# Optimization experiments

Measured on AMD Instinct MI355X. Metric: run time of the kernel, lower is better.

Reference implementation:

```python
import jax, jax.numpy as jnp
import numpy as np

B, N, DIM = 8, 8192, 512
H, DH = 8, 64
INNER = H * DH
EPS = 1e-5


def setup_inputs() -> dict:
    key = jax.random.key(0)
    ks = jax.random.split(key, 5)
    x = jax.random.normal(ks[0], (B, N, DIM), dtype=jnp.float32)
    w_qkv = jax.random.normal(ks[1], (DIM, 3 * INNER), dtype=jnp.float32) * (DIM ** -0.5)
    ln_w = jnp.ones((INNER,), dtype=jnp.float32)
    ln_b = jnp.zeros((INNER,), dtype=jnp.float32)
    w_out = jax.random.normal(ks[2], (INNER, DIM), dtype=jnp.float32) * (INNER ** -0.5)
    b_out = jnp.zeros((DIM,), dtype=jnp.float32)
    return {"x": x, "w_qkv": w_qkv, "ln_w": ln_w, "ln_b": ln_b,
            "w_out": w_out, "b_out": b_out}


def _layernorm(x, w, b):
    mu = jnp.mean(x, axis=-1, keepdims=True)
    var = jnp.mean(jnp.square(x - mu), axis=-1, keepdims=True)
    return (x - mu) * jax.lax.rsqrt(var + EPS) * w + b


def reference(x, w_qkv, ln_w, ln_b, w_out, b_out):
    b, n, _ = x.shape
    qkv = x @ w_qkv  # [b, n, 3*inner]
    q, k, v = jnp.split(qkv, 3, axis=-1)
    # b n (h d) -> b h n d
    def heads(t):
        return t.reshape(b, n, H, DH).transpose(0, 2, 1, 3)
    q, k, v = heads(q), heads(k), heads(v)
    q = jax.nn.relu(q)
    k = jax.nn.relu(k)
    kv = jnp.einsum('bhnm,bhnd->bhmd', k, v)   # [b, h, d, d]
    out = jnp.einsum('bhnm,bhmd->bhnd', q, kv)  # [b, h, n, d]
    out = out.transpose(0, 2, 1, 3).reshape(b, n, INNER)
    out = _layernorm(out, ln_w, ln_b)
    return out @ w_out + b_out
```

## Files before the change

kernel.cpp:

```cpp
#include <hip/hip_runtime.h>
#include <stdint.h>

#define B_ 8
#define N_ 8192
#define DIM_ 512
#define H_ 8
#define DH_ 64
#define ROWS (B_*N_)
#define TRIPLE (3*DIM_)
#define EPS_ 1e-5f
#define PLANE ((size_t)ROWS * 64)

typedef __attribute__((ext_vector_type(8))) short short8;
typedef __attribute__((ext_vector_type(4))) float f32x4;
typedef __attribute__((ext_vector_type(4))) float fl4;
typedef __attribute__((ext_vector_type(4))) unsigned short us4;
typedef __attribute__((ext_vector_type(8))) unsigned short us8;

#define AS1 __attribute__((address_space(1)))
#define AS3 __attribute__((address_space(3)))

__device__ __forceinline__ void gld16(const void* g, void* l) {
    __builtin_amdgcn_global_load_lds((const AS1 void*)(uintptr_t)g,
                                     (AS3 void*)(unsigned)(uintptr_t)l, 16, 0, 0);
}

__device__ inline unsigned short f2bf(float f) {
    union { float f; unsigned int u; } x; x.f = f;
    unsigned int r = x.u + 0x7fffu + ((x.u >> 16) & 1u);
    return (unsigned short)(r >> 16);
}
__device__ inline float bf2f(unsigned short b) {
    union { unsigned int u; float f; } x; x.u = ((unsigned int)b) << 16;
    return x.f;
}

__device__ __forceinline__ int eoff(int row, int col) {
    return row * 64 + (col ^ ((((unsigned)row >> 2) & 3) << 4));
}

__device__ __forceinline__ int aoff(int row, int col) {
    return row * 512 + ((((col >> 3) ^ (row & 7)) << 3) | (col & 7));
}

__global__ __launch_bounds__(256) void k_cvt(const float* __restrict__ x,
                                             unsigned short* __restrict__ xb) {
    size_t i = ((size_t)blockIdx.x * 256 + threadIdx.x) * 8;
    fl4 a = *(const fl4*)(x + i);
    fl4 b = *(const fl4*)(x + i + 4);
    us8 r;
    r[0] = f2bf(a[0]); r[1] = f2bf(a[1]); r[2] = f2bf(a[2]); r[3] = f2bf(a[3]);
    r[4] = f2bf(b[0]); r[5] = f2bf(b[1]); r[6] = f2bf(b[2]); r[7] = f2bf(b[3]);
    *(us8*)(xb + i) = r;
}

__global__ __launch_bounds__(256) void k_prep(const float* __restrict__ wq,
        const float* __restrict__ wo,
        unsigned short* __restrict__ wqT, unsigned short* __restrict__ woT) {
    __shared__ float T[32][33];
    int bid = blockIdx.x;
    const float* src; unsigned short* dst; int srcCols, dstCols, k0, n0;
    if (bid < 768) {
        int tn = bid % 48, tk = bid / 48;
        src = wq; dst = wqT; srcCols = 1536; dstCols = 512;
        k0 = tk * 32; n0 = tn * 32;
    } else {
        int b = bid - 768;
        int tn = b % 16, tk = b / 16;
        src = wo; dst = woT; srcCols = 512; dstCols = 512;
        k0 = tk * 32; n0 = tn * 32;
    }
    int t = threadIdx.x, r = t >> 3, c4 = (t & 7) * 4;
    fl4 v = *(const fl4*)(src + (size_t)(k0 + r) * srcCols + n0 + c4);
    T[c4 + 0][r] = v[0]; T[c4 + 1][r] = v[1];
    T[c4 + 2][r] = v[2]; T[c4 + 3][r] = v[3];
    __syncthreads();
    us4 o;
    o[0] = f2bf(T[r][c4 + 0]); o[1] = f2bf(T[r][c4 + 1]);
    o[2] = f2bf(T[r][c4 + 2]); o[3] = f2bf(T[r][c4 + 3]);
    *(us4*)(dst + (size_t)(n0 + r) * dstCols + k0 + c4) = o;
}

__global__ __launch_bounds__(512, 4) void k_qkv8(const unsigned short* __restrict__ xb,
        const unsigned short* __restrict__ wT,
        unsigned short* __restrict__ qkv)
{
    __shared__ __align__(1024) unsigned short LDSb[3][12288];

    const int tid  = threadIdx.x;
    const int lane = tid & 63;
    const int wid  = tid >> 6;
    const int wr   = wid >> 1;
    const int wc   = wid & 1;
    const int lr   = lane & 15;

    int id  = blockIdx.x;
    int nid = (id & 7) * 384 + (id >> 3);
    int n0  = (nid % 12) * 128;
    int m0  = (nid / 12) * 256;

    const unsigned short* pA[2];
    const unsigned short* pB1;
    unsigned ldstA[2], ldstB;
#pragma unroll
    for (int j = 0; j < 2; ++j) {
        int s    = tid + j * 512;
        int row  = ((s >> 6) << 4) + ((s >> 2) & 15);
        int colb = ((s & 3) << 4) ^ (((s >> 5) & 1) << 5);
        pA[j] = xb + (size_t)(m0 + row) * 512 + (colb >> 1);
        ldstA[j] = (unsigned)((j * 512 + wid * 64) * 8);
    }
    {
        int s    = tid;
        int row  = ((s >> 6) << 4) + ((s >> 2) & 15);
        int colb = ((s & 3) << 4) ^ (((s >> 5) & 1) << 5);
        pB1 = wT + (size_t)(n0 + row) * 512 + (colb >> 1);
        ldstB = (unsigned)(8192 + wid * 64 * 8);
    }
    const int kg = (lane >> 4) * 8;
    const int lo = lr * 32 + (kg ^ ((lr >> 3) << 4));

    auto STAGE = [&](int t, int slot) {
        gld16(pA[0] + t * 32, (void*)&LDSb[slot][ldstA[0]]);
        gld16(pA[1] + t * 32, (void*)&LDSb[slot][ldstA[1]]);
        gld16(pB1   + t * 32, (void*)&LDSb[slot][ldstB]);
    };

    f32x4 acc[4][4] = {};
    short8 af[4], bfr[4];

    STAGE(0, 0);
    STAGE(1, 1);

#define WAITV(n) asm volatile("s_waitcnt vmcnt(" #n ")" ::: "memory")
#pragma unroll
    for (int t = 0; t < 16; ++t) {
        if (t <= 14) WAITV(3);
        else         WAITV(0);
        __builtin_amdgcn_s_barrier();
        __builtin_amdgcn_sched_barrier(0);

        if (t + 2 < 16) STAGE(t + 2, (t + 2) % 3);

        const unsigned short* L = LDSb[t % 3];
#pragma unroll
        for (int m = 0; m < 4; ++m)
            af[m] = *(const short8*)&L[(wr * 4 + m) * 512 + lo];
#pragma unroll
        for (int n = 0; n < 4; ++n)
            bfr[n] = *(const short8*)&L[8192 + (wc * 4 + n) * 512 + lo];

        __builtin_amdgcn_s_setprio(1);
#pragma unroll
        for (int m = 0; m < 4; ++m)
#pragma unroll
            for (int n = 0; n < 4; ++n)
                acc[m][n] = __builtin_amdgcn_mfma_f32_16x16x32_bf16(af[m], bfr[n], acc[m][n], 0, 0, 0);
        __builtin_amdgcn_s_setprio(0);
    }
#undef WAITV

    __syncthreads();

    unsigned short* S = ((unsigned short*)LDSb) + wid * 4096;
    const bool relu_tile = (n0 < 1024);
#pragma unroll
    for (int m = 0; m < 4; ++m) {
        int rbase = m * 16 + ((lane >> 4) << 2);
#pragma unroll
        for (int n = 0; n < 4; ++n) {
            int col = n * 16 + lr;
#pragma unroll
            for (int r = 0; r < 4; ++r) {
                float v = acc[m][n][r];
                if (relu_tile && v < 0.0f) v = 0.0f;
                S[eoff(rbase + r, col)] = f2bf(v);
            }
        }
    }
    __syncthreads();
    {
        int rsub = lane >> 3, sub = lane & 7;
        size_t grow = (size_t)(m0 + wr * 64);
        unsigned short* pb = qkv + (size_t)((n0 >> 6) + wc) * PLANE;
#pragma unroll
        for (int rd = 0; rd < 8; ++rd) {
            int row = rd * 8 + rsub;
            short8 vv = *(const short8*)&S[eoff(row, sub * 8)];
            *(short8*)(pb + (grow + row) * 64 + sub * 8) = vv;
        }
    }
}

__global__ __launch_bounds__(256) void k_qkv_f(const float* __restrict__ x,
        const unsigned short* __restrict__ wT,
        unsigned short* __restrict__ qkv)
{
    __shared__ unsigned short As[128][40];
    __shared__ unsigned short Bs[128][40];
    int t = threadIdx.x;
    int lane = t & 63, wave = t >> 6;
    int m0 = blockIdx.y * 128;
    int n0 = blockIdx.x * 128;
    int wm = (wave & 1) * 64, wn = (wave >> 1) * 64;
    int lr = lane & 15, kg = (lane >> 4) * 8;

    f32x4 acc[4][4] = {};
    for (int k0 = 0; k0 < DIM_; k0 += 32) {
#pragma unroll
        for (int i = 0; i < 4; ++i) {
            int c = t + 256 * i;
            int r = c >> 3, c4 = (c & 7) * 4;
            fl4 v = *(const fl4*)(x + (size_t)(m0 + r) * DIM_ + k0 + c4);
            unsigned short* dst = &As[r][c4];
            dst[0] = f2bf(v[0]); dst[1] = f2bf(v[1]); dst[2] = f2bf(v[2]); dst[3] = f2bf(v[3]);
        }
#pragma unroll
        for (int i = 0; i < 2; ++i) {
            int c = t + 256 * i;
            int r = c >> 2, c8 = (c & 3) * 8;
            *(int4*)&Bs[r][c8] = *(const int4*)(wT + (size_t)(n0 + r) * DIM_ + k0 + c8);
        }
        __syncthreads();
        short8 af[4], bfr[4];
#pragma unroll
        for (int i = 0; i < 4; ++i) af[i]  = *(short8*)&As[wm + i*16 + lr][kg];
#pragma unroll
        for (int j = 0; j < 4; ++j) bfr[j] = *(short8*)&Bs[wn + j*16 + lr][kg];
#pragma unroll
        for (int i = 0; i < 4; ++i)
#pragma unroll
            for (int j = 0; j < 4; ++j)
                acc[i][j] = __builtin_amdgcn_mfma_f32_16x16x32_bf16(af[i], bfr[j], acc[i][j], 0, 0, 0);
        __syncthreads();
    }
#pragma unroll
    for (int i = 0; i < 4; ++i) {
        int row = m0 + wm + i*16 + (lane >> 4) * 4;
#pragma unroll
        for (int j = 0; j < 4; ++j) {
            int col = n0 + wn + j*16 + (lane & 15);
            bool rl = (col < 1024);
            size_t pbase = (size_t)(col >> 6) * PLANE + (col & 63);
#pragma unroll
            for (int r = 0; r < 4; ++r) {
                float v = acc[i][j][r];
                if (rl && v < 0.0f) v = 0.0f;
                qkv[pbase + (size_t)(row + r) * 64] = f2bf(v);
            }
        }
    }
}

__global__ __launch_bounds__(256) void k_kv(const unsigned short* __restrict__ qkv,
                                            float* __restrict__ kv)
{
    __shared__ unsigned short KT[64][136];
    __shared__ unsigned short VT[64][136];
    __shared__ float red[64 * 64];
    int t = threadIdx.x, lane = t & 63, wave = t >> 6;
    int bh = blockIdx.x;
    int b = bh >> 3, h = bh & 7;
    int chunk = blockIdx.y;
    size_t rowbase = (size_t)b * N_ + (size_t)chunk * 1024;
    const unsigned short* kp = qkv + (size_t)(8 + h) * PLANE;
    const unsigned short* vp = qkv + (size_t)(16 + h) * PLANE;
    int lr = lane & 15;

    f32x4 acc[4][4] = {};
    for (int tile = 0; tile < 8; ++tile) {
        size_t r0 = rowbase + tile * 128;
#pragma unroll
        for (int i = 0; i < 2; ++i) {
            int u = t + 256 * i;
            int rp = u >> 3;
            int c8 = (u & 7) * 8;
            size_t ra = r0 + 2 * rp, rb = ra + 1;
            us8 ka = *(const us8*)(kp + ra * 64 + c8);
            us8 kb = *(const us8*)(kp + rb * 64 + c8);
            us8 va = *(const us8*)(vp + ra * 64 + c8);
            us8 vb = *(const us8*)(vp + rb * 64 + c8);
#pragma unroll
            for (int j = 0; j < 8; ++j) {
                int d = c8 + j;
                *(unsigned int*)&KT[d][2 * rp] =
                    (unsigned int)ka[j] | ((unsigned int)kb[j] << 16);
                *(unsigned int*)&VT[d][2 * rp] =
                    (unsigned int)va[j] | ((unsigned int)vb[j] << 16);
            }
        }
        __syncthreads();
        int kg = wave * 32 + (lane >> 4) * 8;
        short8 af[4], bfr[4];
#pragma unroll
        for (int i = 0; i < 4; ++i) af[i]  = *(short8*)&KT[i*16 + lr][kg];
#pragma unroll
        for (int j = 0; j < 4; ++j) bfr[j] = *(short8*)&VT[j*16 + lr][kg];
#pragma unroll
        for (int i = 0; i < 4; ++i)
#pragma unroll
            for (int j = 0; j < 4; ++j)
                acc[i][j] = __builtin_amdgcn_mfma_f32_16x16x32_bf16(af[i], bfr[j], acc[i][j], 0, 0, 0);
        __syncthreads();
    }
    for (int w = 0; w < 4; ++w) {
        if (wave == w) {
#pragma unroll
            for (int i = 0; i < 4; ++i)
#pragma unroll
                for (int j = 0; j < 4; ++j)
#pragma unroll
                    for (int r = 0; r < 4; ++r) {
                        int m = i*16 + (lane >> 4) * 4 + r;
                        int d = j*16 + (lane & 15);
                        if (w == 0) red[m * 64 + d] = acc[i][j][r];
                        else        red[m * 64 + d] += acc[i][j][r];
                    }
        }
        __syncthreads();
    }
    float* kvout = kv + (size_t)bh * 4096;
#pragma unroll
    for (int i = 0; i < 16; ++i) {
        int idx = t + 256 * i;
        atomicAdd(&kvout[idx], red[idx]);
    }
}

__global__ __launch_bounds__(256) void k_kvt(const float* __restrict__ kv,
                                             unsigned short* __restrict__ kvtb) {
    __shared__ float T[64][65];
    int bh = blockIdx.x, t = threadIdx.x;
    const float* src = kv + (size_t)bh * 4096;
    unsigned short* dst = kvtb + (size_t)bh * 4096;
#pragma unroll
    for (int i = 0; i < 16; ++i) {
        int idx = t + 256 * i;
        T[idx & 63][idx >> 6] = src[idx];
    }
    __syncthreads();
#pragma unroll
    for (int i = 0; i < 16; ++i) {
        int idx = t + 256 * i;
        dst[idx] = f2bf(T[idx >> 6][idx & 63]);
    }
}

__global__ __launch_bounds__(512, 2) void k_ao(
        const unsigned short* __restrict__ qkv,
        const unsigned short* __restrict__ kvtb,
        const float* __restrict__ lnw, const float* __restrict__ lnb,
        const unsigned short* __restrict__ woutT,
        const float* __restrict__ bout, float* __restrict__ out)
{
    __shared__ unsigned short attnS[128 * 512];
    __shared__ float lwS[512], lbS[512], muS[128], rsS[128];
    int t = threadIdx.x, lane = t & 63, wave = t >> 6;
    int lr = lane & 15;
    size_t r0 = (size_t)blockIdx.x * 128;
    int b = (int)(r0 / N_);

    for (int i = t; i < 512; i += 512) { lwS[i] = lnw[i]; lbS[i] = lnb[i]; }

    float s4[4] = {}, ss4[4] = {};

#pragma unroll
    for (int h = 0; h < H_; ++h) {
        const unsigned short* qp  = qkv + (size_t)h * PLANE;
        const unsigned short* kvh = kvtb + (size_t)(b * 8 + h) * 4096;
        f32x4 acc[4] = {};
#pragma unroll
        for (int ks = 0; ks < 2; ++ks) {
            int kg = ks * 32 + (lane >> 4) * 8;
            short8 af, bfr[4];
            af = *(const short8*)(qp + (r0 + wave * 16 + lr) * 64 + kg);
#pragma unroll
            for (int j = 0; j < 4; ++j)
                bfr[j] = *(const short8*)(kvh + (j * 16 + lr) * 64 + kg);
#pragma unroll
            for (int j = 0; j < 4; ++j)
                acc[j] = __builtin_amdgcn_mfma_f32_16x16x32_bf16(af, bfr[j], acc[j], 0, 0, 0);
        }
        int rbase = wave * 16 + (lane >> 4) * 4;
#pragma unroll
        for (int j = 0; j < 4; ++j) {
            int col = h * 64 + j * 16 + lr;
#pragma unroll
            for (int r = 0; r < 4; ++r) {
                float v = acc[j][r];
                s4[r] += v;
                ss4[r] += v * v;
                attnS[aoff(rbase + r, col)] = f2bf(v);
            }
        }
    }

#pragma unroll
    for (int q = 0; q < 4; ++q) {
        float s = s4[q], ss = ss4[q];
        s += __shfl_xor(s, 1);  ss += __shfl_xor(ss, 1);
        s += __shfl_xor(s, 2);  ss += __shfl_xor(ss, 2);
        s += __shfl_xor(s, 4);  ss += __shfl_xor(ss, 4);
        s += __shfl_xor(s, 8);  ss += __shfl_xor(ss, 8);
        s4[q] = s; ss4[q] = ss;
    }
    if (lr == 0) {
#pragma unroll
        for (int q = 0; q < 4; ++q) {
            int row = wave * 16 + (lane >> 4) * 4 + q;
            float m = s4[q] * (1.0f / 512.0f);
            muS[row] = m;
            rsS[row] = rsqrtf(ss4[q] * (1.0f / 512.0f) - m * m + EPS_);
        }
    }
    __syncthreads();

    {
        int row = t >> 2, ch = (t & 3) * 16;
        float mm = muS[row], rr = rsS[row];
        unsigned short* base = attnS + row * 512;
#pragma unroll
        for (int g = 0; g < 16; ++g) {
            int colg = ch + g;
            us8* p = (us8*)(base + ((colg ^ (row & 7)) << 3));
            us8 v = *p, o;
#pragma unroll
            for (int j = 0; j < 8; ++j)
                o[j] = f2bf((bf2f(v[j]) - mm) * rr * lwS[colg * 8 + j] + lbS[colg * 8 + j]);
            *p = o;
        }
    }
    __syncthreads();

    {
        int ncol = wave * 64;
#pragma unroll
        for (int half = 0; half < 2; ++half) {
            f32x4 acc[4][4] = {};
            for (int k0 = 0; k0 < 512; k0 += 32) {
                int gk = (k0 >> 3) + (lane >> 4);
                short8 af[4], bfr[4];
#pragma unroll
                for (int m = 0; m < 4; ++m) {
                    int row = half * 64 + m * 16 + lr;
                    af[m] = *(const short8*)&attnS[row * 512 + ((gk ^ (row & 7)) << 3)];
                }
#pragma unroll
                for (int j = 0; j < 4; ++j)
                    bfr[j] = *(const short8*)(woutT + (size_t)(ncol + j * 16 + lr) * 512 + k0 + (lane >> 4) * 8);
#pragma unroll
                for (int m = 0; m < 4; ++m)
#pragma unroll
                    for (int j = 0; j < 4; ++j)
                        acc[m][j] = __builtin_amdgcn_mfma_f32_16x16x32_bf16(af[m], bfr[j], acc[m][j], 0, 0, 0);
            }
#pragma unroll
            for (int m = 0; m < 4; ++m) {
                size_t row = r0 + half * 64 + m * 16 + ((lane >> 4) << 2);
#pragma unroll
                for (int j = 0; j < 4; ++j) {
                    int col = ncol + j * 16 + (lane & 15);
                    float bo = bout[col];
#pragma unroll
                    for (int r = 0; r < 4; ++r)
                        out[(row + r) * DIM_ + col] = acc[m][j][r] + bo;
                }
            }
        }
    }
}

extern "C" void kernel_launch(void* const* d_in, const int* in_sizes, int n_in,
                              void* d_out, int out_size, void* d_ws, size_t ws_size,
                              hipStream_t stream) {
    (void)in_sizes; (void)n_in; (void)out_size;
    const float* x     = (const float*)d_in[0];
    const float* w_qkv = (const float*)d_in[1];
    const float* ln_w  = (const float*)d_in[2];
    const float* ln_b  = (const float*)d_in[3];
    const float* w_out = (const float*)d_in[4];
    const float* b_out = (const float*)d_in[5];
    float* out = (float*)d_out;

    char* ws = (char*)d_ws;
    const size_t QKV_BYTES = (size_t)ROWS * TRIPLE * sizeof(unsigned short);
    const size_t KV_BYTES  = (size_t)64 * 64 * 64 * sizeof(float);
    const size_t WQT_BYTES = (size_t)TRIPLE * DIM_ * sizeof(unsigned short);
    const size_t WOT_BYTES = (size_t)DIM_ * DIM_ * sizeof(unsigned short);
    const size_t KVT_BYTES = (size_t)64 * 64 * 64 * sizeof(unsigned short);
    const size_t XB_BYTES  = (size_t)ROWS * DIM_ * sizeof(unsigned short);
    unsigned short* qkv   = (unsigned short*)ws;
    float*          kvbuf = (float*)(ws + QKV_BYTES);
    unsigned short* wqkvT = (unsigned short*)(ws + QKV_BYTES + KV_BYTES);
    unsigned short* woutT = (unsigned short*)(ws + QKV_BYTES + KV_BYTES + WQT_BYTES);
    unsigned short* kvtb  = (unsigned short*)(ws + QKV_BYTES + KV_BYTES + WQT_BYTES + WOT_BYTES);
    unsigned short* xb    = (unsigned short*)(ws + QKV_BYTES + KV_BYTES + WQT_BYTES + WOT_BYTES + KVT_BYTES);
    const size_t NEED = QKV_BYTES + KV_BYTES + WQT_BYTES + WOT_BYTES + KVT_BYTES + XB_BYTES;

    hipMemsetAsync(kvbuf, 0, KV_BYTES, stream);
    k_prep<<<1024, 256, 0, stream>>>(w_qkv, w_out, wqkvT, woutT);
    if (ws_size >= NEED) {
        k_cvt<<<16384, 256, 0, stream>>>(x, xb);
        k_qkv8<<<dim3(3072), 512, 0, stream>>>(xb, wqkvT, qkv);
    } else {
        k_qkv_f<<<dim3(12, 512), 256, 0, stream>>>(x, wqkvT, qkv);
    }
    k_kv<<<dim3(64, 8), 256, 0, stream>>>(qkv, kvbuf);
    k_kvt<<<64, 256, 0, stream>>>(kvbuf, kvtb);
    k_ao<<<512, 512, 0, stream>>>(qkv, kvtb, ln_w, ln_b, woutT, b_out, out);
}
```

Baseline: 508.9 us.

## Halve k_ao row tile and split heads across waves to raise occupancy

The k_ao block now covers 64 rows instead of 128, which halves the LDS tile to 64KB, and the grid grows to 1024 blocks. The 8 waves are split into 4 row groups times 2 head halves. Each wave writes partial LayerNorm sums to shared memory, and mean and rstd are computed after the barrier. Launch bounds rise to 4 blocks per SM to get more waves resident for latency hiding. In exchange, each w_out B-fragment is reused across only 64 rows, so global/L2 traffic for woutT doubles, and register pressure under the tighter bound may cause spills.

```diff
diff --git a/kernel.cpp b/kernel.cpp
--- a/kernel.cpp
+++ b/kernel.cpp
@@ -346,18 +346,21 @@
     }
 }
 
-__global__ __launch_bounds__(512, 2) void k_ao(
+__global__ __launch_bounds__(512, 4) void k_ao(
         const unsigned short* __restrict__ qkv,
         const unsigned short* __restrict__ kvtb,
         const float* __restrict__ lnw, const float* __restrict__ lnb,
         const unsigned short* __restrict__ woutT,
         const float* __restrict__ bout, float* __restrict__ out)
 {
-    __shared__ unsigned short attnS[128 * 512];
-    __shared__ float lwS[512], lbS[512], muS[128], rsS[128];
+    __shared__ unsigned short attnS[64 * 512];
+    __shared__ float lwS[512], lbS[512];
+    __shared__ float sP[64][2], ssP[64][2];
     int t = threadIdx.x, lane = t & 63, wave = t >> 6;
     int lr = lane & 15;
-    size_t r0 = (size_t)blockIdx.x * 128;
+    int rb = wave & 3;
+    int hh = wave >> 2;
+    size_t r0 = (size_t)blockIdx.x * 64;
     int b = (int)(r0 / N_);
 
     for (int i = t; i < 512; i += 512) { lwS[i] = lnw[i]; lbS[i] = lnb[i]; }
@@ -365,7 +368,8 @@
     float s4[4] = {}, ss4[4] = {};
 
 #pragma unroll
-    for (int h = 0; h < H_; ++h) {
+    for (int hq = 0; hq < 4; ++hq) {
+        int h = hh * 4 + hq;
         const unsigned short* qp  = qkv + (size_t)h * PLANE;
         const unsigned short* kvh = kvtb + (size_t)(b * 8 + h) * 4096;
         f32x4 acc[4] = {};
@@ -373,7 +377,7 @@
         for (int ks = 0; ks < 2; ++ks) {
             int kg = ks * 32 + (lane >> 4) * 8;
             short8 af, bfr[4];
-            af = *(const short8*)(qp + (r0 + wave * 16 + lr) * 64 + kg);
+            af = *(const short8*)(qp + (r0 + rb * 16 + lr) * 64 + kg);
 #pragma unroll
             for (int j = 0; j < 4; ++j)
                 bfr[j] = *(const short8*)(kvh + (j * 16 + lr) * 64 + kg);
@@ -381,7 +385,7 @@
             for (int j = 0; j < 4; ++j)
                 acc[j] = __builtin_amdgcn_mfma_f32_16x16x32_bf16(af, bfr[j], acc[j], 0, 0, 0);
         }
-        int rbase = wave * 16 + (lane >> 4) * 4;
+        int rbase = rb * 16 + (lane >> 4) * 4;
 #pragma unroll
         for (int j = 0; j < 4; ++j) {
             int col = h * 64 + j * 16 + lr;
@@ -407,20 +411,22 @@
     if (lr == 0) {
 #pragma unroll
         for (int q = 0; q < 4; ++q) {
-            int row = wave * 16 + (lane >> 4) * 4 + q;
-            float m = s4[q] * (1.0f / 512.0f);
-            muS[row] = m;
-            rsS[row] = rsqrtf(ss4[q] * (1.0f / 512.0f) - m * m + EPS_);
+            int row = rb * 16 + (lane >> 4) * 4 + q;
+            sP[row][hh]  = s4[q];
+            ssP[row][hh] = ss4[q];
         }
     }
     __syncthreads();
 
     {
-        int row = t >> 2, ch = (t & 3) * 16;
-        float mm = muS[row], rr = rsS[row];
+        int row = t >> 3, ch = (t & 7) * 8;
+        float s  = sP[row][0] + sP[row][1];
+        float ss = ssP[row][0] + ssP[row][1];
+        float mm = s * (1.0f / 512.0f);
+        float rr = rsqrtf(ss * (1.0f / 512.0f) - mm * mm + EPS_);
         unsigned short* base = attnS + row * 512;
 #pragma unroll
-        for (int g = 0; g < 16; ++g) {
+        for (int g = 0; g < 8; ++g) {
             int colg = ch + g;
             us8* p = (us8*)(base + ((colg ^ (row & 7)) << 3));
             us8 v = *p, o;
@@ -434,37 +440,34 @@
 
     {
         int ncol = wave * 64;
-#pragma unroll
-        for (int half = 0; half < 2; ++half) {
-            f32x4 acc[4][4] = {};
-            for (int k0 = 0; k0 < 512; k0 += 32) {
-                int gk = (k0 >> 3) + (lane >> 4);
-                short8 af[4], bfr[4];
-#pragma unroll
-                for (int m = 0; m < 4; ++m) {
-                    int row = half * 64 + m * 16 + lr;
-                    af[m] = *(const short8*)&attnS[row * 512 + ((gk ^ (row & 7)) << 3)];
-                }
+        f32x4 acc[4][4] = {};
+        for (int k0 = 0; k0 < 512; k0 += 32) {
+            int gk = (k0 >> 3) + (lane >> 4);
+            short8 af[4], bfr[4];
+#pragma unroll
+            for (int m = 0; m < 4; ++m) {
+                int row = m * 16 + lr;
+                af[m] = *(const short8*)&attnS[row * 512 + ((gk ^ (row & 7)) << 3)];
+            }
+#pragma unroll
+            for (int j = 0; j < 4; ++j)
+                bfr[j] = *(const short8*)(woutT + (size_t)(ncol + j * 16 + lr) * 512 + k0 + (lane >> 4) * 8);
+#pragma unroll
+            for (int m = 0; m < 4; ++m)
 #pragma unroll
                 for (int j = 0; j < 4; ++j)
-                    bfr[j] = *(const short8*)(woutT + (size_t)(ncol + j * 16 + lr) * 512 + k0 + (lane >> 4) * 8);
-#pragma unroll
-                for (int m = 0; m < 4; ++m)
-#pragma unroll
-                    for (int j = 0; j < 4; ++j)
-                        acc[m][j] = __builtin_amdgcn_mfma_f32_16x16x32_bf16(af[m], bfr[j], acc[m][j], 0, 0, 0);
-            }
-#pragma unroll
-            for (int m = 0; m < 4; ++m) {
-                size_t row = r0 + half * 64 + m * 16 + ((lane >> 4) << 2);
-#pragma unroll
-                for (int j = 0; j < 4; ++j) {
-                    int col = ncol + j * 16 + (lane & 15);
-                    float bo = bout[col];
-#pragma unroll
-                    for (int r = 0; r < 4; ++r)
-                        out[(row + r) * DIM_ + col] = acc[m][j][r] + bo;
-                }
+                    acc[m][j] = __builtin_amdgcn_mfma_f32_16x16x32_bf16(af[m], bfr[j], acc[m][j], 0, 0, 0);
+        }
+#pragma unroll
+        for (int m = 0; m < 4; ++m) {
+            size_t row = r0 + m * 16 + ((lane >> 4) << 2);
+#pragma unroll
+            for (int j = 0; j < 4; ++j) {
+                int col = ncol + j * 16 + (lane & 15);
+                float bo = bout[col];
+#pragma unroll
+                for (int r = 0; r < 4; ++r)
+                    out[(row + r) * DIM_ + col] = acc[m][j][r] + bo;
             }
         }
     }
@@ -507,5 +510,5 @@
     }
     k_kv<<<dim3(64, 8), 256, 0, stream>>>(qkv, kvbuf);
     k_kvt<<<64, 256, 0, stream>>>(kvbuf, kvtb);
-    k_ao<<<512, 512, 0, stream>>>(qkv, kvtb, ln_w, ln_b, woutT, b_out, out);
-}
+    k_ao<<<1024, 512, 0, stream>>>(qkv, kvtb, ln_w, ln_b, woutT, b_out, out);
+}
```

New measurement: 500.7 us. Within noise of the previous version (-1.6%).
